# Performance work log

Measured on AMD Instinct MI355X. Metric: run time of the kernel, lower is better.

The kernel has to match this reference:

```python
import jax, jax.numpy as jnp
import numpy as np

N = 4096; E = 32768; S = 64; V = 16; H0 = 64; H1 = 16; STEPS = 3
SQRT3 = float(np.sqrt(3.0))


def _tp(sx, vx, sy, vy):
    # full CG tensor product restricted to paths landing in 0e/1o
    # sx [n,m0], vx [n,m1,3], sy [n,k0], vy [n,k1,3]
    n = sx.shape[0]
    ss = (sx[:, :, None] * sy[:, None, :]).reshape(n, -1)              # 0e x 0e -> 0e
    dd = (jnp.einsum('nmi,nki->nmk', vx, vy) / SQRT3).reshape(n, -1)    # 1o . 1o -> 0e
    sv = (sx[:, :, None, None] * vy[:, None, :, :]).reshape(n, -1, 3)   # 0e x 1o -> 1o
    vs = (vx[:, :, None, :] * sy[:, None, :, None]).reshape(n, -1, 3)   # 1o x 0e -> 1o
    return jnp.concatenate([ss, dd], -1), jnp.concatenate([sv, vs], -2)


def _tpl_gate(sx, vx, sy, vy, ws, b, wv, n0):
    # TensorProductLinearGate: tensor_product -> Linear -> gate
    s_tp, v_tp = _tp(sx, vx, sy, vy)
    s = s_tp @ ws + b                                  # scalars + gate scalars
    v = jnp.einsum('ntd,tm->nmd', v_tp, wv)
    scal = jax.nn.gelu(s[:, :n0])
    gates = jax.nn.sigmoid(s[:, n0:])
    return scal, v * gates[:, :, None]


def _seg_mean(x, idx, n):
    s = jax.ops.segment_sum(x, idx, num_segments=n)
    c = jax.ops.segment_sum(jnp.ones((x.shape[0],), x.dtype), idx, num_segments=n)
    c = jnp.maximum(c, 1.0).reshape((n,) + (1,) * (x.ndim - 1))
    return s / c


def setup_inputs() -> dict:
    key = jax.random.key(0)
    ks = jax.random.split(key, 20)
    f32 = jnp.float32

    def w(k, shape):
        return jax.random.normal(k, shape, f32) / np.sqrt(shape[-2]).astype(np.float32)

    def bias(k, shape):
        return 0.1 * jax.random.normal(k, shape, f32)

    E1 = 2 * (S + V)          # 160: edge block0 TP width
    E2 = H0 + H1              # 80: edge blocks 1-2 TP width
    K0 = H0 + 1; K1 = H1 + 1  # message concat sh
    N0TP = S * K0 + V * K1    # 4432
    N1TP = S * K1 + V * K0    # 2128
    return {
        'node_s': jax.random.normal(ks[0], (N, S), f32),
        'node_v': jax.random.normal(ks[1], (N, V, 3), f32),
        'senders': jax.random.randint(ks[2], (E,), 0, N, jnp.int32),
        'receivers': jax.random.randint(ks[3], (E,), 0, N, jnp.int32),
        'e1_ws': w(ks[4], (STEPS, E1, H0 + H1)),
        'e1_b': bias(ks[5], (STEPS, H0 + H1)),
        'e1_wv': w(ks[6], (STEPS, E1, H1)),
        'e2_ws': w(ks[7], (STEPS, 2, E2, H0 + H1)),
        'e2_b': bias(ks[8], (STEPS, 2, H0 + H1)),
        'e2_wv': w(ks[9], (STEPS, 2, E2, H1)),
        'n_ws': w(ks[10], (STEPS, 3, N0TP, S + V)),
        'n_b': bias(ks[11], (STEPS, 3, S + V)),
        'n_wv': w(ks[12], (STEPS, 3, N1TP, V)),
        'l_ws': w(ks[13], (STEPS, S, S)),
        'l_b': bias(ks[14], (STEPS, S)),
        'l_wv': w(ks[15], (STEPS, V, V)),
    }


def reference(node_s, node_v, senders, receivers, e1_ws, e1_b, e1_wv,
              e2_ws, e2_b, e2_wv, n_ws, n_b, n_wv, l_ws, l_b, l_wv):
    norm = float(E - 1)
    for step in range(STEPS):
        s_i, v_i = node_s[senders], node_v[senders]
        s_j, v_j = node_s[receivers], node_v[receivers]
        r = v_i[:, 0] - v_j[:, 0]                    # slice_by_mul[:1] = positions
        rn = jnp.linalg.norm(r, axis=-1, keepdims=True)
        unit = r / jnp.maximum(rn, 1e-9)
        a_s = jnp.ones((E, 1), node_s.dtype)          # Y_0, component norm
        a_v = (SQRT3 * unit)[:, None, :]              # Y_1, component norm
        m_s = jnp.concatenate([s_i, s_j], -1)
        m_v = jnp.concatenate([v_i, v_j], -2)
        for blk in range(3):
            if blk == 0:
                ws, b, wv = e1_ws[step], e1_b[step], e1_wv[step]
            else:
                ws, b, wv = e2_ws[step, blk - 1], e2_b[step, blk - 1], e2_wv[step, blk - 1]
            m_s, m_v = _tpl_gate(m_s, m_v, a_s, a_v, ws, b, wv, H0)
        # ---- aggregate (segment_mean) + normalize_messages ----
        ms = _seg_mean(m_s, receivers, N) / norm
        mv = _seg_mean(m_v, receivers, N) / norm
        as_ = _seg_mean(a_s, receivers, N) / norm
        av = _seg_mean(a_v, receivers, N) / norm
        y_s = jnp.concatenate([ms, as_], -1)          # [N, H0+1]
        y_v = jnp.concatenate([mv, av], -2)           # [N, H1+1, 3]
        for blk in range(3):
            node_s, node_v = _tpl_gate(node_s, node_v, y_s, y_v,
                                       n_ws[step, blk], n_b[step, blk], n_wv[step, blk], S)
        # ---- final per-step Linear(irreps_in) ----
        node_s = node_s @ l_ws[step] + l_b[step]
        node_v = jnp.einsum('nmd,mk->nkd', node_v, l_wv[step])
    return jnp.concatenate([node_v.reshape(node_v.shape[0], -1), node_s], -1)
```

## Files before the change

kernel.cpp:

```cpp
#include <hip/hip_runtime.h>
#include <math.h>

constexpr int NND = 4096;
constexpr int EDG = 32768;
constexpr float SQRT3  = 1.7320508075688772f;
constexpr float ISQRT3 = 0.5773502691896258f;
constexpr float NORMI  = 1.0f / 32767.0f;

__device__ __forceinline__ float gelu_f(float x) {
    float x3 = x * x * x;
    return 0.5f * x * (1.0f + tanhf(0.7978845608028654f * (x + 0.044715f * x3)));
}
__device__ __forceinline__ float sigmoid_f(float x) {
    return 1.0f / (1.0f + expf(-x));
}

__global__ __launch_bounds__(256)
void segnn_deg_kernel(const int* __restrict__ rcv, int* __restrict__ deg) {
    const int e = blockIdx.x * 256 + threadIdx.x;
    if (e < EDG) atomicAdd(deg + rcv[e], 1);
}

__global__ __launch_bounds__(1024)
void segnn_scan_kernel(const int* __restrict__ deg, int* __restrict__ off) {
    __shared__ int tots[1024];
    const int t = threadIdx.x;
    const int v0 = deg[4*t], v1 = deg[4*t+1], v2 = deg[4*t+2], v3 = deg[4*t+3];
    const int p1 = v0, p2 = p1 + v1, p3 = p2 + v2, p4 = p3 + v3;
    tots[t] = p4;
    __syncthreads();
    for (int d = 1; d < 1024; d <<= 1) {
        const int add = (t >= d) ? tots[t - d] : 0;
        __syncthreads();
        tots[t] += add;
        __syncthreads();
    }
    const int excl = t ? tots[t-1] : 0;
    off[4*t+0] = excl;
    off[4*t+1] = excl + p1;
    off[4*t+2] = excl + p2;
    off[4*t+3] = excl + p3;
    if (t == 1023) off[4096] = tots[1023];
}

__global__ __launch_bounds__(256)
void segnn_scatter_kernel(const int* __restrict__ rcv, const int* __restrict__ off,
                          int* __restrict__ cursor, int* __restrict__ elist) {
    const int e = blockIdx.x * 256 + threadIdx.x;
    if (e < EDG) {
        const int j = rcv[e];
        const int p = atomicAdd(cursor + j, 1);
        elist[off[j] + p] = e;
    }
}

template<int NSX, int NVX>
__device__ __forceinline__ void edge_phase_w(
    const int lane,
    const float* __restrict__ Ws, const float* __restrict__ Bs,
    const float* __restrict__ Wv,
    float (*xt)[10], float (*x2)[10], float (*cb)[96], float (*cvv)[48])
{
    const int cs = lane & 15, kg = lane >> 4;
    constexpr int KA = NSX + NVX;
    constexpr int CH = KA / 4;

    {
        float acc[8][6];
#pragma unroll
        for (int j = 0; j < 8; ++j)
#pragma unroll
            for (int c = 0; c < 6; ++c) acc[j][c] = 0.0f;
        const int r0 = kg * CH;
#pragma unroll 4
        for (int rr = 0; rr < CH; ++rr) {
            const int r = r0 + rr;
            const float* wp = Ws + r*80 + cs;
            const float w0 = wp[0], w1 = wp[16], w2 = wp[32], w3 = wp[48], w4 = wp[64];
            const float w5 = (r < NSX) ? Wv[r*16 + cs] : 0.0f;
            const float2 xa = *reinterpret_cast<const float2*>(&xt[r][0]);
            const float2 xb = *reinterpret_cast<const float2*>(&xt[r][2]);
            const float2 xc = *reinterpret_cast<const float2*>(&xt[r][4]);
            const float2 xd = *reinterpret_cast<const float2*>(&xt[r][6]);
            const float xe[8] = { xa.x,xa.y, xb.x,xb.y, xc.x,xc.y, xd.x,xd.y };
#pragma unroll
            for (int j = 0; j < 8; ++j) {
                acc[j][0] = fmaf(xe[j], w0, acc[j][0]);
                acc[j][1] = fmaf(xe[j], w1, acc[j][1]);
                acc[j][2] = fmaf(xe[j], w2, acc[j][2]);
                acc[j][3] = fmaf(xe[j], w3, acc[j][3]);
                acc[j][4] = fmaf(xe[j], w4, acc[j][4]);
                acc[j][5] = fmaf(xe[j], w5, acc[j][5]);
            }
        }
#pragma unroll
        for (int j = 0; j < 8; ++j)
#pragma unroll
            for (int c = 0; c < 6; ++c) {
                float a = acc[j][c];
                a += __shfl_xor(a, 16);
                a += __shfl_xor(a, 32);
                acc[j][c] = a;
            }
        if (lane < 16) {
#pragma unroll
            for (int j = 0; j < 8; ++j) {
#pragma unroll
                for (int c = 0; c < 5; ++c) cb[j][cs + 16*c] = acc[j][c] + Bs[cs + 16*c];
                cb[j][80 + cs] = acc[j][5];
            }
        }
    }

    {
        constexpr int CHB = NVX / 4;
        float av[8][3];
#pragma unroll
        for (int j = 0; j < 8; ++j) { av[j][0]=0.0f; av[j][1]=0.0f; av[j][2]=0.0f; }
        const int m0 = kg * CHB;
#pragma unroll
        for (int mm = 0; mm < CHB; ++mm) {
            const int m = m0 + mm;
            const float w = Wv[(NSX + m)*16 + cs];
#pragma unroll
            for (int d = 0; d < 3; ++d) {
                const float2 xa = *reinterpret_cast<const float2*>(&x2[d*NVX + m][0]);
                const float2 xb = *reinterpret_cast<const float2*>(&x2[d*NVX + m][2]);
                const float2 xc = *reinterpret_cast<const float2*>(&x2[d*NVX + m][4]);
                const float2 xd = *reinterpret_cast<const float2*>(&x2[d*NVX + m][6]);
                const float xe[8] = { xa.x,xa.y, xb.x,xb.y, xc.x,xc.y, xd.x,xd.y };
#pragma unroll
                for (int j = 0; j < 8; ++j) av[j][d] = fmaf(xe[j], w, av[j][d]);
            }
        }
#pragma unroll
        for (int j = 0; j < 8; ++j)
#pragma unroll
            for (int d = 0; d < 3; ++d) {
                float a = av[j][d];
                a += __shfl_xor(a, 16);
                a += __shfl_xor(a, 32);
                av[j][d] = a;
            }
        if (lane < 16) {
#pragma unroll
            for (int j = 0; j < 8; ++j)
#pragma unroll
                for (int d = 0; d < 3; ++d) cvv[j][cs*3 + d] = av[j][d];
        }
    }
    asm volatile("" ::: "memory");
}

__global__ __launch_bounds__(256, 2)
void segnn_edge_fused(const float* __restrict__ cs, const float* __restrict__ cv,
                      const int* __restrict__ snd, const int* __restrict__ rcv,
                      const float* __restrict__ W0s, const float* __restrict__ B0, const float* __restrict__ W0v,
                      const float* __restrict__ W1s, const float* __restrict__ B1, const float* __restrict__ W1v,
                      const float* __restrict__ W2s, const float* __restrict__ B2, const float* __restrict__ W2v,
                      float* __restrict__ msg) {
    __shared__ __align__(16) float XT [4][160][10];
    __shared__ __align__(16) float X2T[4][96][10];
    __shared__ __align__(16) float Cb [4][8][96];
    __shared__ __align__(16) float Cv [4][8][48];
    __shared__ float UU [4][8][4];

    const int tid  = threadIdx.x;
    const int w    = tid >> 6;
    const int lane = tid & 63;
    const int e0   = blockIdx.x * 32 + w * 8;

    float (*xt)[10]  = XT[w];
    float (*x2)[10]  = X2T[w];
    float (*cb)[96]  = Cb[w];
    float (*cvv)[48] = Cv[w];
    float (*uuw)[4]  = UU[w];

#pragma unroll
    for (int it = 0; it < 16; ++it) {
        const int e = it >> 1, half = it & 1;
        const int node = (half ? rcv : snd)[e0 + e];
        xt[half*64 + lane][e] = cs[(size_t)node*64 + lane];
    }
#pragma unroll
    for (int it = 0; it < 16; ++it) {
        const int e = it >> 1, half = it & 1;
        if (lane < 48) {
            const int node = (half ? rcv : snd)[e0 + e];
            const int m = lane / 3, d = lane - 3*m;
            x2[d*32 + half*16 + m][e] = cv[(size_t)node*48 + lane];
        }
    }
    asm volatile("" ::: "memory");
    if (lane < 8) {
        const float rx = x2[0][lane]  - x2[16][lane];
        const float ry = x2[32][lane] - x2[48][lane];
        const float rz = x2[64][lane] - x2[80][lane];
        const float rinv = 1.0f / fmaxf(sqrtf(rx*rx+ry*ry+rz*rz), 1e-9f);
        uuw[lane][0] = rx*rinv; uuw[lane][1] = ry*rinv; uuw[lane][2] = rz*rinv;
    }
    asm volatile("" ::: "memory");
#pragma unroll
    for (int it = 0; it < 4; ++it) {
        const int idx = it*64 + lane;
        const int e = idx >> 5, mm = idx & 31;
        xt[128 + mm][e] = x2[mm][e]*uuw[e][0] + x2[32+mm][e]*uuw[e][1] + x2[64+mm][e]*uuw[e][2];
    }
    asm volatile("" ::: "memory");

    edge_phase_w<128,32>(lane, W0s, B0, W0v, xt, x2, cb, cvv);
#pragma unroll
    for (int it = 0; it < 8; ++it) {
        xt[lane][it] = gelu_f(cb[it][lane]);
    }
#pragma unroll
    for (int it = 0; it < 2; ++it) {
        const int idx = it*64 + lane;
        const int e = idx >> 4, o = idx & 15;
        const float g = sigmoid_f(cb[e][64+o]);
        const float t = cb[e][80+o] * SQRT3;
        float p = 0.0f;
#pragma unroll
        for (int d = 0; d < 3; ++d) {
            const float vd = fmaf(t, uuw[e][d], cvv[e][o*3+d]) * g;
            x2[d*16 + o][e] = vd;
            p = fmaf(vd, uuw[e][d], p);
        }
        xt[64 + o][e] = p;
    }
    asm volatile("" ::: "memory");

    edge_phase_w<64,16>(lane, W1s, B1, W1v, xt, x2, cb, cvv);
#pragma unroll
    for (int it = 0; it < 8; ++it) {
        xt[lane][it] = gelu_f(cb[it][lane]);
    }
#pragma unroll
    for (int it = 0; it < 2; ++it) {
        const int idx = it*64 + lane;
        const int e = idx >> 4, o = idx & 15;
        const float g = sigmoid_f(cb[e][64+o]);
        const float t = cb[e][80+o] * SQRT3;
        float p = 0.0f;
#pragma unroll
        for (int d = 0; d < 3; ++d) {
            const float vd = fmaf(t, uuw[e][d], cvv[e][o*3+d]) * g;
            x2[d*16 + o][e] = vd;
            p = fmaf(vd, uuw[e][d], p);
        }
        xt[64 + o][e] = p;
    }
    asm volatile("" ::: "memory");

    edge_phase_w<64,16>(lane, W2s, B2, W2v, xt, x2, cb, cvv);
#pragma unroll
    for (int it = 0; it < 15; ++it) {
        const int idx = it*64 + lane;
        if (idx < 920) {
            const int e = idx / 115, f = idx - 115*e;
            float vv;
            if (f < 64) {
                vv = gelu_f(cb[e][f]);
            } else if (f < 112) {
                const int q = f - 64, o = q / 3, d = q - 3*o;
                const float g = sigmoid_f(cb[e][64+o]);
                vv = fmaf(cb[e][80+o] * SQRT3, uuw[e][d], cvv[e][q]) * g;
            } else {
                vv = uuw[e][f-112];
            }
            msg[(size_t)(e0+e)*116 + f] = vv;
        }
    }
}

__global__ __launch_bounds__(128)
void segnn_gather_kernel(const float* __restrict__ msg, const int* __restrict__ off,
                         const int* __restrict__ elist,
                         float* __restrict__ y_s, float* __restrict__ y_v) {
    const int n = blockIdx.x, f = threadIdx.x;
    const int o0 = off[n], o1 = off[n+1];
    const int deg = o1 - o0;
    float acc = 0.0f;
    for (int p = o0; p < o1; ++p) {
        const int eid = elist[p];
        if (f < 115) acc += msg[(size_t)eid*116 + f];
    }
    const float inv = NORMI / (float)(deg > 0 ? deg : 1);
    if (f < 64)        y_s[(size_t)n*65 + f] = acc * inv;
    else if (f < 112)  y_v[(size_t)n*51 + (f-64)] = acc * inv;
    else if (f < 115)  y_v[(size_t)n*51 + 48 + (f-112)] = SQRT3 * acc * inv;
    else if (f == 115) y_s[(size_t)n*65 + 64] = deg ? NORMI : 0.0f;
}

__global__ __launch_bounds__(512, 4)
void segnn_node_kernel(const float* __restrict__ in_s, const float* __restrict__ in_v,
                       const float* __restrict__ y_s, const float* __restrict__ y_v,
                       const float* __restrict__ W,  const float* __restrict__ B,
                       const float* __restrict__ Wv,
                       float* __restrict__ out_s, float* __restrict__ out_v) {
    __shared__ __align__(16) float xsL[8*66];
    __shared__ __align__(16) float ysL[8*68];
    __shared__ __align__(16) float xvL[8*49];
    __shared__ __align__(16) float yvL[8*52];
    __shared__ __align__(16) float Xa[2][3072];
    __shared__ __align__(16) float red[4][16][41];
    __shared__ float finGG[8*16];

    const int tid  = threadIdx.x;
    const int lane = tid & 63;
    const int wv   = tid >> 6;
    const int nb0  = blockIdx.x * 8;

    for (int idx = tid; idx < 8*64; idx += 512) { const int n = idx >> 6, m = idx & 63; xsL[n*66+m] = in_s[(size_t)(nb0+n)*64 + m]; }
    for (int idx = tid; idx < 8*65; idx += 512) { const int n = idx / 65, k = idx - n*65; ysL[n*68+k] = y_s[(size_t)(nb0+n)*65 + k]; }
    for (int idx = tid; idx < 8*48; idx += 512) { const int n = idx / 48, m = idx - n*48; xvL[n*49+m] = in_v[(size_t)(nb0+n)*48 + m]; }
    for (int idx = tid; idx < 8*51; idx += 512) { const int n = idx / 51, m = idx - n*51; yvL[n*52+m] = y_v[(size_t)(nb0+n)*51 + m]; }
    __syncthreads();

    {
        const int cs = tid & 15;
        const int rowgrp = tid >> 4;

        float acc[8][5];
#pragma unroll
        for (int n = 0; n < 8; ++n)
#pragma unroll
            for (int c = 0; c < 5; ++c) acc[n][c] = 0.0f;

        auto genS = [&](int t, int b) {
            const int base = t * 128;
#pragma unroll
            for (int ii = 0; ii < 2; ++ii) {
                const int idx = tid + ii*512;
                const int rl = idx >> 3, n = idx & 7;
                const int r = base + rl;
                float val = 0.0f;
                if (r < 4160) {
                    const int m = r / 65, k = r - m*65;
                    val = xsL[n*66+m] * ysL[n*68+k];
                } else if (r < 4432) {
                    const int q = r - 4160;
                    const int m = q / 17, k = q - m*17;
                    val = (xvL[n*49+m*3+0]*yvL[n*52+k*3+0] +
                           xvL[n*49+m*3+1]*yvL[n*52+k*3+1] +
                           xvL[n*49+m*3+2]*yvL[n*52+k*3+2]) * ISQRT3;
                }
                Xa[b][idx] = val;
            }
        };

        genS(0, 0);
        __syncthreads();
        for (int t = 0; t < 35; ++t) {
            if (t + 1 < 35) genS(t + 1, (t + 1) & 1);
            const int base = t * 128;
            const float* Xb = &Xa[t & 1][0];
#pragma unroll
            for (int v2 = 0; v2 < 4; ++v2) {
                const int rl = rowgrp + 32*v2;
                const int r  = base + rl;
                const int wr = r < 4431 ? r : 4431;
                const float* wp = W + (size_t)wr * 80 + cs;
                const float w0 = wp[0], w1 = wp[16], w2 = wp[32], w3 = wp[48], w4_ = wp[64];
                const float4 xq0 = *reinterpret_cast<const float4*>(&Xb[rl*8]);
                const float4 xq1 = *reinterpret_cast<const float4*>(&Xb[rl*8+4]);
                const float xn[8] = { xq0.x, xq0.y, xq0.z, xq0.w, xq1.x, xq1.y, xq1.z, xq1.w };
#pragma unroll
                for (int n = 0; n < 8; ++n) {
                    acc[n][0] = fmaf(xn[n], w0,  acc[n][0]);
                    acc[n][1] = fmaf(xn[n], w1,  acc[n][1]);
                    acc[n][2] = fmaf(xn[n], w2,  acc[n][2]);
                    acc[n][3] = fmaf(xn[n], w3,  acc[n][3]);
                    acc[n][4] = fmaf(xn[n], w4_, acc[n][4]);
                }
            }
            __syncthreads();
        }

#pragma unroll
        for (int n = 0; n < 8; ++n)
#pragma unroll
            for (int c = 0; c < 5; ++c) {
                float a = acc[n][c];
                a += __shfl_xor(a, 16);
                a += __shfl_xor(a, 32);
                acc[n][c] = a;
            }
        if (lane < 16 && wv < 4) {
#pragma unroll
            for (int n = 0; n < 8; ++n)
#pragma unroll
                for (int c = 0; c < 5; ++c) red[wv][lane][n*5+c] = acc[n][c];
        }
        __syncthreads();
        if (lane < 16 && wv >= 4) {
#pragma unroll
            for (int n = 0; n < 8; ++n)
#pragma unroll
                for (int c = 0; c < 5; ++c) red[wv-4][lane][n*5+c] += acc[n][c];
        }
        __syncthreads();
        for (int idx = tid; idx < 8*80; idx += 512) {
            const int n = idx / 80, col = idx - n*80;
            const int cs2 = col & 15, ci2 = col >> 4;
            float s = B[col];
#pragma unroll
            for (int ww = 0; ww < 4; ++ww) s += red[ww][cs2][n*5+ci2];
            if (col < 64) out_s[(size_t)(nb0+n)*64 + col] = gelu_f(s);
            else          finGG[n*16 + (col-64)] = s;
        }
        __syncthreads();
    }

    {
        const int j4 = tid & 3;
        const int ngrp = (tid >> 2) & 1;
        const int rg = tid >> 3;

        float av[12][4];
#pragma unroll
        for (int a = 0; a < 12; ++a)
#pragma unroll
            for (int c = 0; c < 4; ++c) av[a][c] = 0.0f;

        auto genV = [&](int t, int b) {
            const int base = t * 128;
#pragma unroll
            for (int ii = 0; ii < 6; ++ii) {
                const int idx = tid + ii*512;
                const int rl = idx / 24, ar = idx - rl*24;
                const int n = ar / 3, d = ar - n*3;
                const int r = base + rl;
                float val = 0.0f;
                if (r < 1088) {
                    const int m = r / 17, k = r - m*17;
                    val = xsL[n*66+m] * yvL[n*52+k*3+d];
                } else if (r < 2128) {
                    const int q = r - 1088;
                    const int m = q / 65, k = q - m*65;
                    val = xvL[n*49+m*3+d] * ysL[n*68+k];
                }
                Xa[b][idx] = val;
            }
        };

        genV(0, 0);
        __syncthreads();
        for (int t = 0; t < 17; ++t) {
            if (t + 1 < 17) genV(t + 1, (t + 1) & 1);
            const float* Xb = &Xa[t & 1][0];
#pragma unroll
            for (int v2 = 0; v2 < 2; ++v2) {
                const int rl = rg + 64*v2;
                const int r  = t*128 + rl;
                const int wr = r < 2127 ? r : 2127;
                const float4 w4 = *reinterpret_cast<const float4*>(&Wv[(size_t)wr*16 + 4*j4]);
                const float4 xq0 = *reinterpret_cast<const float4*>(&Xb[rl*24 + 12*ngrp]);
                const float4 xq1 = *reinterpret_cast<const float4*>(&Xb[rl*24 + 12*ngrp + 4]);
                const float4 xq2 = *reinterpret_cast<const float4*>(&Xb[rl*24 + 12*ngrp + 8]);
                const float xr[12] = { xq0.x,xq0.y,xq0.z,xq0.w, xq1.x,xq1.y,xq1.z,xq1.w, xq2.x,xq2.y,xq2.z,xq2.w };
#pragma unroll
                for (int a = 0; a < 12; ++a) {
                    av[a][0] = fmaf(xr[a], w4.x, av[a][0]);
                    av[a][1] = fmaf(xr[a], w4.y, av[a][1]);
                    av[a][2] = fmaf(xr[a], w4.z, av[a][2]);
                    av[a][3] = fmaf(xr[a], w4.w, av[a][3]);
                }
            }
            __syncthreads();
        }

        float* redf = &red[0][0][0];
#pragma unroll
        for (int a = 0; a < 12; ++a)
#pragma unroll
            for (int c = 0; c < 4; ++c) {
                float x = av[a][c];
                x += __shfl_xor(x, 8);
                x += __shfl_xor(x, 16);
                x += __shfl_xor(x, 32);
                av[a][c] = x;
            }
        if (lane < 8 && wv < 4) {
#pragma unroll
            for (int a = 0; a < 12; ++a)
#pragma unroll
                for (int c = 0; c < 4; ++c) redf[wv*392 + lane*49 + a*4 + c] = av[a][c];
        }
        __syncthreads();
        if (lane < 8 && wv >= 4) {
#pragma unroll
            for (int a = 0; a < 12; ++a)
#pragma unroll
                for (int c = 0; c < 4; ++c) redf[(wv-4)*392 + lane*49 + a*4 + c] += av[a][c];
        }
        __syncthreads();
        for (int idx = tid; idx < 24*16; idx += 512) {
            const int ar = idx >> 4, j = idx & 15;
            const int n = ar / 3, d = ar - n*3;
            const int ng2 = ar / 12, a2 = ar - 12*ng2;
            const int jj4 = j >> 2, c2 = j & 3;
            float s = 0.0f;
#pragma unroll
            for (int ww = 0; ww < 4; ++ww) s += redf[ww*392 + (jj4 + 4*ng2)*49 + a2*4 + c2];
            out_v[(size_t)(nb0+n)*48 + j*3 + d] = s * sigmoid_f(finGG[n*16 + j]);
        }
    }
}

__global__ __launch_bounds__(256)
void segnn_linear_kernel(const float* __restrict__ in_s, const float* __restrict__ in_v,
                         const float* __restrict__ lws, const float* __restrict__ lb,
                         const float* __restrict__ lwv,
                         float* __restrict__ out_s, float* __restrict__ out_v,
                         float* __restrict__ out_cat) {
    const int idx = blockIdx.x * 256 + threadIdx.x;
    if (idx >= NND * 112) return;
    const int nidx = idx / 112, f = idx - nidx * 112;
    if (f < 48) {
        const int k = f / 3, d = f - 3*k;
        const float* vp = in_v + (size_t)nidx * 48 + d;
        float acc = 0.0f;
#pragma unroll
        for (int m = 0; m < 16; ++m) acc = fmaf(vp[m*3], lwv[m*16 + k], acc);
        if (out_cat) out_cat[(size_t)nidx*112 + f] = acc;
        else         out_v[(size_t)nidx*48 + f] = acc;
    } else {
        const int o = f - 48;
        const float* sp = in_s + (size_t)nidx * 64;
        float acc = lb[o];
#pragma unroll
        for (int m = 0; m < 64; ++m) acc = fmaf(sp[m], lws[m*64 + o], acc);
        if (out_cat) out_cat[(size_t)nidx*112 + f] = acc;
        else         out_s[(size_t)nidx*64 + o] = acc;
    }
}

extern "C" void kernel_launch(void* const* d_in, const int* in_sizes, int n_in,
                              void* d_out, int out_size, void* d_ws, size_t ws_size,
                              hipStream_t stream) {
    const float* in_s  = (const float*)d_in[0];
    const float* in_v  = (const float*)d_in[1];
    const int*   snd   = (const int*)  d_in[2];
    const int*   rcv   = (const int*)  d_in[3];
    const float* e1_ws = (const float*)d_in[4];
    const float* e1_b  = (const float*)d_in[5];
    const float* e1_wv = (const float*)d_in[6];
    const float* e2_ws = (const float*)d_in[7];
    const float* e2_b  = (const float*)d_in[8];
    const float* e2_wv = (const float*)d_in[9];
    const float* n_ws  = (const float*)d_in[10];
    const float* n_b   = (const float*)d_in[11];
    const float* n_wv  = (const float*)d_in[12];
    const float* l_ws  = (const float*)d_in[13];
    const float* l_b   = (const float*)d_in[14];
    const float* l_wv  = (const float*)d_in[15];

    float* ws    = (float*)d_ws;
    float* cur_s = ws;
    float* cur_v = cur_s + 262144;
    float* nxt_s = cur_v + 196608;
    float* nxt_v = nxt_s + 262144;
    float* y_s   = nxt_v + 196608;
    float* y_v   = y_s + 266240;
    float* msg   = y_v + 208896;
    int*   deg    = (int*)(msg + 3801088);
    int*   cursor = deg + 4096;
    int*   off    = cursor + 4096;
    int*   elist  = off + 4097;

    hipMemsetAsync(deg, 0, (size_t)8192 * sizeof(int), stream);
    hipMemcpyAsync(cur_s, in_s, (size_t)262144 * sizeof(float), hipMemcpyDeviceToDevice, stream);
    hipMemcpyAsync(cur_v, in_v, (size_t)196608 * sizeof(float), hipMemcpyDeviceToDevice, stream);
    segnn_deg_kernel<<<EDG/256, 256, 0, stream>>>(rcv, deg);
    segnn_scan_kernel<<<1, 1024, 0, stream>>>(deg, off);
    segnn_scatter_kernel<<<EDG/256, 256, 0, stream>>>(rcv, off, cursor, elist);

    for (int step = 0; step < 3; ++step) {
        segnn_edge_fused<<<EDG/32, 256, 0, stream>>>(cur_s, cur_v, snd, rcv,
            e1_ws + (size_t)step*160*80, e1_b + step*80, e1_wv + (size_t)step*160*16,
            e2_ws + (size_t)(step*2+0)*80*80, e2_b + (step*2+0)*80, e2_wv + (size_t)(step*2+0)*80*16,
            e2_ws + (size_t)(step*2+1)*80*80, e2_b + (step*2+1)*80, e2_wv + (size_t)(step*2+1)*80*16,
            msg);
        segnn_gather_kernel<<<NND, 128, 0, stream>>>(msg, off, elist, y_s, y_v);

        segnn_node_kernel<<<NND/8, 512, 0, stream>>>(cur_s, cur_v, y_s, y_v,
            n_ws + (size_t)(step*3+0)*4432*80, n_b + (step*3+0)*80, n_wv + (size_t)(step*3+0)*2128*16,
            nxt_s, nxt_v);
        segnn_node_kernel<<<NND/8, 512, 0, stream>>>(nxt_s, nxt_v, y_s, y_v,
            n_ws + (size_t)(step*3+1)*4432*80, n_b + (step*3+1)*80, n_wv + (size_t)(step*3+1)*2128*16,
            cur_s, cur_v);
        segnn_node_kernel<<<NND/8, 512, 0, stream>>>(cur_s, cur_v, y_s, y_v,
            n_ws + (size_t)(step*3+2)*4432*80, n_b + (step*3+2)*80, n_wv + (size_t)(step*3+2)*2128*16,
            nxt_s, nxt_v);

        segnn_linear_kernel<<<(NND*112 + 255)/256, 256, 0, stream>>>(nxt_s, nxt_v,
            l_ws + (size_t)step*64*64, l_b + step*64, l_wv + (size_t)step*16*16,
            cur_s, cur_v, (step == 2) ? (float*)d_out : nullptr);
    }
}
```

Baseline: 1.074 ms.

## Split node kernel reduction dimension across two blocks with combine kernel

Each node block of 8 nodes now runs as two blocks, each covering half of the tensor-product rows (K split) for both the scalar and vector GEMMs. The blocks write partial sums to scratch reused from the message buffer. A new combine kernel adds the halves, applies the bias, gelu and sigmoid gating. This doubles grid size (512 to 1024 blocks) for better CU occupancy on the large GPU, at the cost of an extra kernel launch and a partial-sum round trip through memory per node block.

```diff
diff --git a/kernel.cpp b/kernel.cpp
--- a/kernel.cpp
+++ b/kernel.cpp
@@ -295,21 +295,20 @@
 __global__ __launch_bounds__(512, 4)
 void segnn_node_kernel(const float* __restrict__ in_s, const float* __restrict__ in_v,
                        const float* __restrict__ y_s, const float* __restrict__ y_v,
-                       const float* __restrict__ W,  const float* __restrict__ B,
-                       const float* __restrict__ Wv,
-                       float* __restrict__ out_s, float* __restrict__ out_v) {
+                       const float* __restrict__ W,  const float* __restrict__ Wv,
+                       float* __restrict__ ps, float* __restrict__ pv) {
     __shared__ __align__(16) float xsL[8*66];
     __shared__ __align__(16) float ysL[8*68];
     __shared__ __align__(16) float xvL[8*49];
     __shared__ __align__(16) float yvL[8*52];
-    __shared__ __align__(16) float Xa[2][3072];
+    __shared__ __align__(16) float Xa[2][2048];
     __shared__ __align__(16) float red[4][16][41];
-    __shared__ float finGG[8*16];
 
     const int tid  = threadIdx.x;
     const int lane = tid & 63;
     const int wv   = tid >> 6;
-    const int nb0  = blockIdx.x * 8;
+    const int nb0  = (blockIdx.x >> 1) * 8;
+    const int kb   = blockIdx.x & 1;
 
     for (int idx = tid; idx < 8*64; idx += 512) { const int n = idx >> 6, m = idx & 63; xsL[n*66+m] = in_s[(size_t)(nb0+n)*64 + m]; }
     for (int idx = tid; idx < 8*65; idx += 512) { const int n = idx / 65, k = idx - n*65; ysL[n*68+k] = y_s[(size_t)(nb0+n)*65 + k]; }
@@ -320,6 +319,7 @@
     {
         const int cs = tid & 15;
         const int rowgrp = tid >> 4;
+        const int rbase = kb * 2216, rend = rbase + 2216;
 
         float acc[8][5];
 #pragma unroll
@@ -328,22 +328,24 @@
             for (int c = 0; c < 5; ++c) acc[n][c] = 0.0f;
 
         auto genS = [&](int t, int b) {
-            const int base = t * 128;
+            const int tb = rbase + t * 128;
 #pragma unroll
             for (int ii = 0; ii < 2; ++ii) {
                 const int idx = tid + ii*512;
                 const int rl = idx >> 3, n = idx & 7;
-                const int r = base + rl;
+                const int r = tb + rl;
                 float val = 0.0f;
-                if (r < 4160) {
-                    const int m = r / 65, k = r - m*65;
-                    val = xsL[n*66+m] * ysL[n*68+k];
-                } else if (r < 4432) {
-                    const int q = r - 4160;
-                    const int m = q / 17, k = q - m*17;
-                    val = (xvL[n*49+m*3+0]*yvL[n*52+k*3+0] +
-                           xvL[n*49+m*3+1]*yvL[n*52+k*3+1] +
-                           xvL[n*49+m*3+2]*yvL[n*52+k*3+2]) * ISQRT3;
+                if (r < rend) {
+                    if (r < 4160) {
+                        const int m = r / 65, k = r - m*65;
+                        val = xsL[n*66+m] * ysL[n*68+k];
+                    } else {
+                        const int q = r - 4160;
+                        const int m = q / 17, k = q - m*17;
+                        val = (xvL[n*49+m*3+0]*yvL[n*52+k*3+0] +
+                               xvL[n*49+m*3+1]*yvL[n*52+k*3+1] +
+                               xvL[n*49+m*3+2]*yvL[n*52+k*3+2]) * ISQRT3;
+                    }
                 }
                 Xa[b][idx] = val;
             }
@@ -351,14 +353,14 @@
 
         genS(0, 0);
         __syncthreads();
-        for (int t = 0; t < 35; ++t) {
-            if (t + 1 < 35) genS(t + 1, (t + 1) & 1);
-            const int base = t * 128;
+        for (int t = 0; t < 18; ++t) {
+            if (t + 1 < 18) genS(t + 1, (t + 1) & 1);
+            const int tb = rbase + t * 128;
             const float* Xb = &Xa[t & 1][0];
 #pragma unroll
             for (int v2 = 0; v2 < 4; ++v2) {
                 const int rl = rowgrp + 32*v2;
-                const int r  = base + rl;
+                const int r  = tb + rl;
                 const int wr = r < 4431 ? r : 4431;
                 const float* wp = W + (size_t)wr * 80 + cs;
                 const float w0 = wp[0], w1 = wp[16], w2 = wp[32], w3 = wp[48], w4_ = wp[64];
@@ -403,11 +405,10 @@
         for (int idx = tid; idx < 8*80; idx += 512) {
             const int n = idx / 80, col = idx - n*80;
             const int cs2 = col & 15, ci2 = col >> 4;
-            float s = B[col];
+            float s = 0.0f;
 #pragma unroll
             for (int ww = 0; ww < 4; ++ww) s += red[ww][cs2][n*5+ci2];
-            if (col < 64) out_s[(size_t)(nb0+n)*64 + col] = gelu_f(s);
-            else          finGG[n*16 + (col-64)] = s;
+            ps[((size_t)kb*NND + nb0 + n)*80 + col] = s;
         }
         __syncthreads();
     }
@@ -416,6 +417,7 @@
         const int j4 = tid & 3;
         const int ngrp = (tid >> 2) & 1;
         const int rg = tid >> 3;
+        const int rbase = kb * 1064, rend = rbase + 1064;
 
         float av[12][4];
 #pragma unroll
@@ -424,21 +426,23 @@
             for (int c = 0; c < 4; ++c) av[a][c] = 0.0f;
 
         auto genV = [&](int t, int b) {
-            const int base = t * 128;
-#pragma unroll
-            for (int ii = 0; ii < 6; ++ii) {
+            const int tb = rbase + t * 64;
+#pragma unroll
+            for (int ii = 0; ii < 3; ++ii) {
                 const int idx = tid + ii*512;
                 const int rl = idx / 24, ar = idx - rl*24;
                 const int n = ar / 3, d = ar - n*3;
-                const int r = base + rl;
+                const int r = tb + rl;
                 float val = 0.0f;
-                if (r < 1088) {
-                    const int m = r / 17, k = r - m*17;
-                    val = xsL[n*66+m] * yvL[n*52+k*3+d];
-                } else if (r < 2128) {
-                    const int q = r - 1088;
-                    const int m = q / 65, k = q - m*65;
-                    val = xvL[n*49+m*3+d] * ysL[n*68+k];
+                if (r < rend) {
+                    if (r < 1088) {
+                        const int m = r / 17, k = r - m*17;
+                        val = xsL[n*66+m] * yvL[n*52+k*3+d];
+                    } else {
+                        const int q = r - 1088;
+                        const int m = q / 65, k = q - m*65;
+                        val = xvL[n*49+m*3+d] * ysL[n*68+k];
+                    }
                 }
                 Xa[b][idx] = val;
             }
@@ -449,10 +453,9 @@
         for (int t = 0; t < 17; ++t) {
             if (t + 1 < 17) genV(t + 1, (t + 1) & 1);
             const float* Xb = &Xa[t & 1][0];
-#pragma unroll
-            for (int v2 = 0; v2 < 2; ++v2) {
-                const int rl = rg + 64*v2;
-                const int r  = t*128 + rl;
+            {
+                const int rl = rg;
+                const int r  = rbase + t*64 + rl;
                 const int wr = r < 2127 ? r : 2127;
                 const float4 w4 = *reinterpret_cast<const float4*>(&Wv[(size_t)wr*16 + 4*j4]);
                 const float4 xq0 = *reinterpret_cast<const float4*>(&Xb[rl*24 + 12*ngrp]);
@@ -503,8 +506,26 @@
             float s = 0.0f;
 #pragma unroll
             for (int ww = 0; ww < 4; ++ww) s += redf[ww*392 + (jj4 + 4*ng2)*49 + a2*4 + c2];
-            out_v[(size_t)(nb0+n)*48 + j*3 + d] = s * sigmoid_f(finGG[n*16 + j]);
-        }
+            pv[((size_t)kb*NND + nb0 + n)*48 + j*3 + d] = s;
+        }
+    }
+}
+
+__global__ __launch_bounds__(256)
+void segnn_combine_kernel(const float* __restrict__ ps, const float* __restrict__ pv,
+                          const float* __restrict__ B,
+                          float* __restrict__ out_s, float* __restrict__ out_v) {
+    const int idx = blockIdx.x * 256 + threadIdx.x;
+    if (idx >= NND * 112) return;
+    const int n = idx / 112, f = idx - n * 112;
+    if (f < 64) {
+        const float s = ps[(size_t)n*80 + f] + ps[((size_t)NND + n)*80 + f] + B[f];
+        out_s[(size_t)n*64 + f] = gelu_f(s);
+    } else {
+        const int q = f - 64, o = q / 3;
+        const float graw = ps[(size_t)n*80 + 64 + o] + ps[((size_t)NND + n)*80 + 64 + o] + B[64 + o];
+        const float v = pv[(size_t)n*48 + q] + pv[((size_t)NND + n)*48 + q];
+        out_v[(size_t)n*48 + q] = v * sigmoid_f(graw);
     }
 }
 
@@ -569,6 +590,9 @@
     int*   off    = cursor + 4096;
     int*   elist  = off + 4097;
 
+    float* ps = msg;
+    float* pv = msg + 655360;
+
     hipMemsetAsync(deg, 0, (size_t)8192 * sizeof(int), stream);
     hipMemcpyAsync(cur_s, in_s, (size_t)262144 * sizeof(float), hipMemcpyDeviceToDevice, stream);
     hipMemcpyAsync(cur_v, in_v, (size_t)196608 * sizeof(float), hipMemcpyDeviceToDevice, stream);
@@ -576,6 +600,7 @@
     segnn_scan_kernel<<<1, 1024, 0, stream>>>(deg, off);
     segnn_scatter_kernel<<<EDG/256, 256, 0, stream>>>(rcv, off, cursor, elist);
 
+    const int cgrid = (NND*112 + 255) / 256;
     for (int step = 0; step < 3; ++step) {
         segnn_edge_fused<<<EDG/32, 256, 0, stream>>>(cur_s, cur_v, snd, rcv,
             e1_ws + (size_t)step*160*80, e1_b + step*80, e1_wv + (size_t)step*160*16,
@@ -584,17 +609,19 @@
             msg);
         segnn_gather_kernel<<<NND, 128, 0, stream>>>(msg, off, elist, y_s, y_v);
 
-        segnn_node_kernel<<<NND/8, 512, 0, stream>>>(cur_s, cur_v, y_s, y_v,
-            n_ws + (size_t)(step*3+0)*4432*80, n_b + (step*3+0)*80, n_wv + (size_t)(step*3+0)*2128*16,
-            nxt_s, nxt_v);
-        segnn_node_kernel<<<NND/8, 512, 0, stream>>>(nxt_s, nxt_v, y_s, y_v,
-            n_ws + (size_t)(step*3+1)*4432*80, n_b + (step*3+1)*80, n_wv + (size_t)(step*3+1)*2128*16,
-            cur_s, cur_v);
-        segnn_node_kernel<<<NND/8, 512, 0, stream>>>(cur_s, cur_v, y_s, y_v,
-            n_ws + (size_t)(step*3+2)*4432*80, n_b + (step*3+2)*80, n_wv + (size_t)(step*3+2)*2128*16,
-            nxt_s, nxt_v);
-
-        segnn_linear_kernel<<<(NND*112 + 255)/256, 256, 0, stream>>>(nxt_s, nxt_v,
+        segnn_node_kernel<<<NND/4, 512, 0, stream>>>(cur_s, cur_v, y_s, y_v,
+            n_ws + (size_t)(step*3+0)*4432*80, n_wv + (size_t)(step*3+0)*2128*16, ps, pv);
+        segnn_combine_kernel<<<cgrid, 256, 0, stream>>>(ps, pv, n_b + (step*3+0)*80, nxt_s, nxt_v);
+
+        segnn_node_kernel<<<NND/4, 512, 0, stream>>>(nxt_s, nxt_v, y_s, y_v,
+            n_ws + (size_t)(step*3+1)*4432*80, n_wv + (size_t)(step*3+1)*2128*16, ps, pv);
+        segnn_combine_kernel<<<cgrid, 256, 0, stream>>>(ps, pv, n_b + (step*3+1)*80, cur_s, cur_v);
+
+        segnn_node_kernel<<<NND/4, 512, 0, stream>>>(cur_s, cur_v, y_s, y_v,
+            n_ws + (size_t)(step*3+2)*4432*80, n_wv + (size_t)(step*3+2)*2128*16, ps, pv);
+        segnn_combine_kernel<<<cgrid, 256, 0, stream>>>(ps, pv, n_b + (step*3+2)*80, nxt_s, nxt_v);
+
+        segnn_linear_kernel<<<cgrid, 256, 0, stream>>>(nxt_s, nxt_v,
             l_ws + (size_t)step*64*64, l_b + step*64, l_wv + (size_t)step*16*16,
             cur_s, cur_v, (step == 2) ? (float*)d_out : nullptr);
     }
```

Measured after the change: 2.344 ms. 118% more time.

## Give each wave private K-slices and LDS buffers, removing block barriers in node GEMM

Applied to the files above, without the earlier changes.

The node kernel's TP-to-Linear reductions no longer stream shared 128-row tiles through a double buffer guarded by __syncthreads. Each wave now owns a contiguous slice of the contraction rows (554 scalar, 266 vector) and a private XOR-swizzled LDS buffer, so it generates and consumes its own tile with only compiler fences. This removes dozens of block-wide barriers per kernel and reduces LDS bank conflicts. In exchange it drops the generate/consume double-buffer overlap and depends on wave-lockstep execution for the within-wave write-then-read, since only compiler fences order those accesses.

```diff
diff --git a/kernel.cpp b/kernel.cpp
--- a/kernel.cpp
+++ b/kernel.cpp
@@ -302,7 +302,7 @@
     __shared__ __align__(16) float ysL[8*68];
     __shared__ __align__(16) float xvL[8*49];
     __shared__ __align__(16) float yvL[8*52];
-    __shared__ __align__(16) float Xa[2][3072];
+    __shared__ __align__(16) float Xw[8][1024];
     __shared__ __align__(16) float red[4][16][41];
     __shared__ float finGG[8*16];
 
@@ -317,9 +317,18 @@
     for (int idx = tid; idx < 8*51; idx += 512) { const int n = idx / 51, m = idx - n*51; yvL[n*52+m] = y_v[(size_t)(nb0+n)*51 + m]; }
     __syncthreads();
 
+    float* Xp = &Xw[wv][0];
+
     {
-        const int cs = tid & 15;
-        const int rowgrp = tid >> 4;
+        const int cs = lane & 15;
+        const int g  = lane >> 4;
+        const int gj = lane >> 3;
+        const int gn = lane & 7;
+        const int wbase = wv * 554;
+        const float* xsn = xsL + gn*66;
+        const float* ysn = ysL + gn*68;
+        const float* xvn = xvL + gn*49;
+        const float* yvn = yvL + gn*52;
 
         float acc[8][5];
 #pragma unroll
@@ -327,43 +336,38 @@
 #pragma unroll
             for (int c = 0; c < 5; ++c) acc[n][c] = 0.0f;
 
-        auto genS = [&](int t, int b) {
-            const int base = t * 128;
-#pragma unroll
-            for (int ii = 0; ii < 2; ++ii) {
-                const int idx = tid + ii*512;
-                const int rl = idx >> 3, n = idx & 7;
-                const int r = base + rl;
+        for (int c = 0; c < 9; ++c) {
+            const int cb64 = c * 64;
+#pragma unroll
+            for (int j = 0; j < 8; ++j) {
+                const int rl = gj + 8*j;
+                const int rloc = cb64 + rl;
                 float val = 0.0f;
-                if (r < 4160) {
-                    const int m = r / 65, k = r - m*65;
-                    val = xsL[n*66+m] * ysL[n*68+k];
-                } else if (r < 4432) {
-                    const int q = r - 4160;
-                    const int m = q / 17, k = q - m*17;
-                    val = (xvL[n*49+m*3+0]*yvL[n*52+k*3+0] +
-                           xvL[n*49+m*3+1]*yvL[n*52+k*3+1] +
-                           xvL[n*49+m*3+2]*yvL[n*52+k*3+2]) * ISQRT3;
+                if (rloc < 554) {
+                    const int r = wbase + rloc;
+                    if (r < 4160) {
+                        const int m = r / 65, k = r - m*65;
+                        val = xsn[m] * ysn[k];
+                    } else {
+                        const int q = r - 4160;
+                        const int m = q / 17, k = q - m*17;
+                        val = (xvn[m*3+0]*yvn[k*3+0] + xvn[m*3+1]*yvn[k*3+1] +
+                               xvn[m*3+2]*yvn[k*3+2]) * ISQRT3;
+                    }
                 }
-                Xa[b][idx] = val;
-            }
-        };
-
-        genS(0, 0);
-        __syncthreads();
-        for (int t = 0; t < 35; ++t) {
-            if (t + 1 < 35) genS(t + 1, (t + 1) & 1);
-            const int base = t * 128;
-            const float* Xb = &Xa[t & 1][0];
-#pragma unroll
-            for (int v2 = 0; v2 < 4; ++v2) {
-                const int rl = rowgrp + 32*v2;
-                const int r  = base + rl;
-                const int wr = r < 4431 ? r : 4431;
+                Xp[(lane + 64*j) ^ ((((gj + 8*j) >> 4) & 3) << 3)] = val;
+            }
+            asm volatile("" ::: "memory");
+#pragma unroll 8
+            for (int i = 0; i < 16; ++i) {
+                const int rl = g*16 + i;
+                const int r  = wbase + cb64 + rl;
+                const int wr = r < 4432 ? r : 4431;
                 const float* wp = W + (size_t)wr * 80 + cs;
                 const float w0 = wp[0], w1 = wp[16], w2 = wp[32], w3 = wp[48], w4_ = wp[64];
-                const float4 xq0 = *reinterpret_cast<const float4*>(&Xb[rl*8]);
-                const float4 xq1 = *reinterpret_cast<const float4*>(&Xb[rl*8+4]);
+                const int sb = (rl*8) ^ (g << 3);
+                const float4 xq0 = *reinterpret_cast<const float4*>(&Xp[sb]);
+                const float4 xq1 = *reinterpret_cast<const float4*>(&Xp[sb+4]);
                 const float xn[8] = { xq0.x, xq0.y, xq0.z, xq0.w, xq1.x, xq1.y, xq1.z, xq1.w };
 #pragma unroll
                 for (int n = 0; n < 8; ++n) {
@@ -374,7 +378,7 @@
                     acc[n][4] = fmaf(xn[n], w4_, acc[n][4]);
                 }
             }
-            __syncthreads();
+            asm volatile("" ::: "memory");
         }
 
 #pragma unroll
@@ -413,9 +417,13 @@
     }
 
     {
-        const int j4 = tid & 3;
-        const int ngrp = (tid >> 2) & 1;
-        const int rg = tid >> 3;
+        const int j4   = lane & 3;
+        const int ngrp = (lane >> 2) & 1;
+        const int rg   = lane >> 3;
+        const int q    = lane & 31;
+        const int gl   = lane >> 5;
+        const int qn   = q / 3, qd = q - 3*qn;
+        const int wbase = wv * 266;
 
         float av[12][4];
 #pragma unroll
@@ -423,41 +431,40 @@
 #pragma unroll
             for (int c = 0; c < 4; ++c) av[a][c] = 0.0f;
 
-        auto genV = [&](int t, int b) {
-            const int base = t * 128;
-#pragma unroll
-            for (int ii = 0; ii < 6; ++ii) {
-                const int idx = tid + ii*512;
-                const int rl = idx / 24, ar = idx - rl*24;
-                const int n = ar / 3, d = ar - n*3;
-                const int r = base + rl;
-                float val = 0.0f;
-                if (r < 1088) {
-                    const int m = r / 17, k = r - m*17;
-                    val = xsL[n*66+m] * yvL[n*52+k*3+d];
-                } else if (r < 2128) {
-                    const int q = r - 1088;
-                    const int m = q / 65, k = q - m*65;
-                    val = xvL[n*49+m*3+d] * ysL[n*68+k];
+        for (int c = 0; c < 9; ++c) {
+            const int cb32 = c * 32;
+#pragma unroll 4
+            for (int j = 0; j < 16; ++j) {
+                const int rl = gl + 2*j;
+                if (q < 24) {
+                    const int rloc = cb32 + rl;
+                    float val = 0.0f;
+                    if (rloc < 266) {
+                        const int r = wbase + rloc;
+                        if (r < 1088) {
+                            const int m = r / 17, k = r - m*17;
+                            val = xsL[qn*66+m] * yvL[qn*52+k*3+qd];
+                        } else {
+                            const int t2 = r - 1088;
+                            const int m = t2 / 65, k = t2 - m*65;
+                            val = xvL[qn*49+m*3+qd] * ysL[qn*68+k];
+                        }
+                    }
+                    Xp[(rl*32 + q) ^ ((rl & 7) << 2)] = val;
                 }
-                Xa[b][idx] = val;
-            }
-        };
-
-        genV(0, 0);
-        __syncthreads();
-        for (int t = 0; t < 17; ++t) {
-            if (t + 1 < 17) genV(t + 1, (t + 1) & 1);
-            const float* Xb = &Xa[t & 1][0];
-#pragma unroll
-            for (int v2 = 0; v2 < 2; ++v2) {
-                const int rl = rg + 64*v2;
-                const int r  = t*128 + rl;
-                const int wr = r < 2127 ? r : 2127;
+            }
+            asm volatile("" ::: "memory");
+#pragma unroll
+            for (int i = 0; i < 4; ++i) {
+                const int rl = rg + 8*i;
+                const int r  = wbase + cb32 + rl;
+                const int wr = r < 2128 ? r : 2127;
                 const float4 w4 = *reinterpret_cast<const float4*>(&Wv[(size_t)wr*16 + 4*j4]);
-                const float4 xq0 = *reinterpret_cast<const float4*>(&Xb[rl*24 + 12*ngrp]);
-                const float4 xq1 = *reinterpret_cast<const float4*>(&Xb[rl*24 + 12*ngrp + 4]);
-                const float4 xq2 = *reinterpret_cast<const float4*>(&Xb[rl*24 + 12*ngrp + 8]);
+                const int xb = rl*32 + 12*ngrp;
+                const int xo = (rl & 7) << 2;
+                const float4 xq0 = *reinterpret_cast<const float4*>(&Xp[(xb)     ^ xo]);
+                const float4 xq1 = *reinterpret_cast<const float4*>(&Xp[(xb + 4) ^ xo]);
+                const float4 xq2 = *reinterpret_cast<const float4*>(&Xp[(xb + 8) ^ xo]);
                 const float xr[12] = { xq0.x,xq0.y,xq0.z,xq0.w, xq1.x,xq1.y,xq1.z,xq1.w, xq2.x,xq2.y,xq2.z,xq2.w };
 #pragma unroll
                 for (int a = 0; a < 12; ++a) {
@@ -467,7 +474,7 @@
                     av[a][3] = fmaf(xr[a], w4.w, av[a][3]);
                 }
             }
-            __syncthreads();
+            asm volatile("" ::: "memory");
         }
 
         float* redf = &red[0][0][0];
```

Result: slower. 1.242 ms (+15.7%).
